# Performance work log

Measured on AMD Instinct MI355X. Metric: run time of the kernel, lower is better.

Reference implementation:

```python
import jax, jax.numpy as jnp
import numpy as np

EPS = 1e-06

def elu_feature_map(x):
    return jax.nn.elu(x) + 1.0

def setup_inputs() -> dict:
    key = jax.random.key(0)
    k1, k2, k3 = jax.random.split(key, 3)
    B, N, H, D = 4, 8192, 8, 64
    queries = jax.random.normal(k1, (B, N, H, D), dtype=jnp.float32)
    keys = jax.random.normal(k2, (B, N, H, D), dtype=jnp.float32)
    values = jax.random.normal(k3, (B, N, H, D), dtype=jnp.float32)
    key_lengths_mask = jnp.ones((B, N), dtype=jnp.float32)  # all keys valid
    return {"queries": queries, "keys": keys, "values": values,
            "key_lengths_mask": key_lengths_mask}

def reference(queries, keys, values, key_lengths_mask):
    # queries/keys/values: [B, N, H, D]; key_lengths_mask: [B, N]
    Q = elu_feature_map(queries)
    K = elu_feature_map(keys) * key_lengths_mask[:, :, None, None]
    # KV: [B, H, M, D] outer-product accumulation over sequence
    KV = jnp.einsum('bnhd,bnhm->bhmd', K, values)
    # normalizer Z: [B, N, H]
    Z = 1.0 / (jnp.einsum('bnhd,bhd->bnh', Q, K.sum(axis=1)) + EPS)
    # output V: [B, N, H, M]
    V = jnp.einsum('bnhd,bhmd,bnh->bnhm', Q, KV, Z)
    return V
```

## Files before the change

### kernel.cpp

```cpp
#include <hip/hip_runtime.h>

static constexpr int B = 4;
static constexpr int N = 8192;
static constexpr int H = 8;
static constexpr int BH = B * H;
#define EPSF 1e-6f

typedef _Float16 f16;
typedef _Float16 f16x8 __attribute__((ext_vector_type(8)));
typedef float f32x4 __attribute__((ext_vector_type(4)));

__device__ __forceinline__ float featmap(float x) {
    return x > 0.0f ? (x + 1.0f) : __expf(x);
}

union H8 { f16x8 v; unsigned long long u[2]; };
__device__ __forceinline__ f16x8 lds_load8(const f16* p) {
    H8 r;
    r.u[0] = *(const unsigned long long*)(p);
    r.u[1] = *(const unsigned long long*)(p + 4);
    return r.v;
}
__device__ __forceinline__ unsigned pack2(float a, float b) {
    union { f16 h[2]; unsigned u; } x;
    x.h[0] = (f16)a; x.h[1] = (f16)b;
    return x.u;
}
__device__ __forceinline__ unsigned long long pack4(float a, float b, float c, float d) {
    union { f16 h[4]; unsigned long long u; } x;
    x.h[0] = (f16)a; x.h[1] = (f16)b; x.h[2] = (f16)c; x.h[3] = (f16)d;
    return x.u;
}

static constexpr int S1 = 16;
static constexpr int ROWS1 = N / S1;
static constexpr int NSTEPS1 = ROWS1 / 32;

__global__ __launch_bounds__(256, 2) void kv_pass(
    const float* __restrict__ keys,
    const float* __restrict__ values,
    const float* __restrict__ mask,
    float* __restrict__ kv,
    float* __restrict__ ksum)
{
    const int bh = blockIdx.x, b = bh >> 3, h = bh & 7;
    const int t = threadIdx.x;
    const int wave = t >> 6, lane = t & 63;
    const int p = t >> 4;
    const int c = t & 15;
    const int quad = lane >> 4;
    const int l15 = lane & 15;
    const int n0 = blockIdx.y * ROWS1;

    __shared__ f16 KT[2][64][36];
    __shared__ f16 VT[2][64][36];
    __shared__ float Ksw[4][64];

    const float* mrow = mask + (size_t)b * N;

    int n = n0 + 2 * p;
    size_t g0 = ((size_t)((b * N + n) * H + h)) * 64 + c * 4;
    size_t g1 = g0 + (size_t)H * 64;
    float4 kq0 = *(const float4*)(keys + g0);
    float4 kq1 = *(const float4*)(keys + g1);
    float4 vq0 = *(const float4*)(values + g0);
    float4 vq1 = *(const float4*)(values + g1);
    float mk0 = mrow[n], mk1 = mrow[n + 1];

    f32x4 acc[4];
    #pragma unroll
    for (int i = 0; i < 4; ++i) acc[i] = (f32x4){0.f, 0.f, 0.f, 0.f};
    float ksacc[4] = {0.f, 0.f, 0.f, 0.f};

    for (int s = 0; s < NSTEPS1; ++s) {
        const int buf = s & 1;
        const float fk0[4] = {featmap(kq0.x) * mk0, featmap(kq0.y) * mk0,
                              featmap(kq0.z) * mk0, featmap(kq0.w) * mk0};
        const float fk1[4] = {featmap(kq1.x) * mk1, featmap(kq1.y) * mk1,
                              featmap(kq1.z) * mk1, featmap(kq1.w) * mk1};
        const float fv0[4] = {vq0.x, vq0.y, vq0.z, vq0.w};
        const float fv1[4] = {vq1.x, vq1.y, vq1.z, vq1.w};
        #pragma unroll
        for (int dd = 0; dd < 4; ++dd) {
            ksacc[dd] += fk0[dd] + fk1[dd];
            *(unsigned*)&KT[buf][c * 4 + dd][2 * p] = pack2(fk0[dd], fk1[dd]);
            *(unsigned*)&VT[buf][c * 4 + dd][2 * p] = pack2(fv0[dd], fv1[dd]);
        }
        if (s + 1 < NSTEPS1) {
            const int nn = n0 + (s + 1) * 32 + 2 * p;
            const size_t h0 = ((size_t)((b * N + nn) * H + h)) * 64 + c * 4;
            const size_t h1 = h0 + (size_t)H * 64;
            kq0 = *(const float4*)(keys + h0);
            kq1 = *(const float4*)(keys + h1);
            vq0 = *(const float4*)(values + h0);
            vq1 = *(const float4*)(values + h1);
            mk0 = mrow[nn]; mk1 = mrow[nn + 1];
        }
        __syncthreads();
        const f16x8 afr = lds_load8(&VT[buf][wave * 16 + l15][quad * 8]);
        #pragma unroll
        for (int dt = 0; dt < 4; ++dt) {
            const f16x8 bfr = lds_load8(&KT[buf][dt * 16 + l15][quad * 8]);
            acc[dt] = __builtin_amdgcn_mfma_f32_16x16x32_f16(afr, bfr, acc[dt], 0, 0, 0);
        }
    }

    float* kvb = kv + (size_t)bh * 4096;
    #pragma unroll
    for (int dt = 0; dt < 4; ++dt) {
        #pragma unroll
        for (int reg = 0; reg < 4; ++reg) {
            const int m = wave * 16 + quad * 4 + reg;
            atomicAdd(kvb + m * 64 + dt * 16 + l15, acc[dt][reg]);
        }
    }
    #pragma unroll
    for (int dd = 0; dd < 4; ++dd) {
        float v = ksacc[dd];
        v += __shfl_xor(v, 16);
        v += __shfl_xor(v, 32);
        if (lane < 16) Ksw[wave][lane * 4 + dd] = v;
    }
    __syncthreads();
    if (t < 64) {
        atomicAdd(ksum + bh * 64 + t, Ksw[0][t] + Ksw[1][t] + Ksw[2][t] + Ksw[3][t]);
    }
}

__global__ __launch_bounds__(256, 2) void out_pass(
    const float* __restrict__ queries,
    const float* __restrict__ kv,
    const float* __restrict__ ksum,
    float* __restrict__ out)
{
    const int bh = blockIdx.x, b = bh >> 3, h = bh & 7;
    const int t = threadIdx.x;
    const int wave = t >> 6, lane = t & 63;
    const int quad = lane >> 4;
    const int l15 = lane & 15;
    const int n0 = blockIdx.y * 256;

    __shared__ f16 Qsh[256][68];
    __shared__ f16 KVh[64][68];
    __shared__ float Ksh[64];

    #pragma unroll
    for (int l = 0; l < 4; ++l) {
        const int idx = t + l * 256;
        const int m = idx >> 4, cc = idx & 15;
        const float4 v = *(const float4*)(kv + (size_t)bh * 4096 + m * 64 + cc * 4);
        *(unsigned long long*)&KVh[m][cc * 4] = pack4(v.x, v.y, v.z, v.w);
    }
    if (t < 64) Ksh[t] = ksum[bh * 64 + t];

    #pragma unroll
    for (int l = 0; l < 16; ++l) {
        const int idx = t + l * 256;
        const int r = idx >> 4, cc = idx & 15;
        const int nn = n0 + r;
        const float4 q = *(const float4*)(queries + ((size_t)((b * N + nn) * H + h)) * 64 + cc * 4);
        *(unsigned long long*)&Qsh[r][cc * 4] =
            pack4(featmap(q.x), featmap(q.y), featmap(q.z), featmap(q.w));
    }
    __syncthreads();

    f16x8 bfr[4][2];
    #pragma unroll
    for (int mt = 0; mt < 4; ++mt)
        #pragma unroll
        for (int ks = 0; ks < 2; ++ks)
            bfr[mt][ks] = lds_load8(&KVh[mt * 16 + l15][ks * 32 + quad * 8]);
    f16x8 bz[2];
    #pragma unroll
    for (int ks = 0; ks < 2; ++ks) {
        #pragma unroll
        for (int j = 0; j < 8; ++j) {
            const float kval = Ksh[ks * 32 + quad * 8 + j];
            bz[ks][j] = (l15 == 0) ? (f16)kval : (f16)0.f;
        }
    }

    #pragma unroll
    for (int nt = 0; nt < 4; ++nt) {
        const int r0 = wave * 64 + nt * 16;
        f32x4 acc[4];
        #pragma unroll
        for (int i = 0; i < 4; ++i) acc[i] = (f32x4){0.f, 0.f, 0.f, 0.f};
        f32x4 az = (f32x4){0.f, 0.f, 0.f, 0.f};

        #pragma unroll
        for (int ks = 0; ks < 2; ++ks) {
            const f16x8 afr = lds_load8(&Qsh[r0 + l15][ks * 32 + quad * 8]);
            #pragma unroll
            for (int mt = 0; mt < 4; ++mt)
                acc[mt] = __builtin_amdgcn_mfma_f32_16x16x32_f16(afr, bfr[mt][ks], acc[mt], 0, 0, 0);
            az = __builtin_amdgcn_mfma_f32_16x16x32_f16(afr, bz[ks], az, 0, 0, 0);
        }

        #pragma unroll
        for (int reg = 0; reg < 4; ++reg) {
            const float den = __shfl(az[reg], lane & 48);
            const float zin = 1.0f / (den + EPSF);
            const int nn = n0 + r0 + quad * 4 + reg;
            float* op = out + ((size_t)((b * N + nn) * H + h)) * 64 + l15;
            #pragma unroll
            for (int mt = 0; mt < 4; ++mt)
                op[mt * 16] = acc[mt][reg] * zin;
        }
    }
}

extern "C" void kernel_launch(void* const* d_in, const int* in_sizes, int n_in,
                              void* d_out, int out_size, void* d_ws, size_t ws_size,
                              hipStream_t stream)
{
    const float* q    = (const float*)d_in[0];
    const float* k    = (const float*)d_in[1];
    const float* v    = (const float*)d_in[2];
    const float* mask = (const float*)d_in[3];
    float* out = (float*)d_out;

    float* kv = (float*)d_ws;
    float* ks = kv + (size_t)BH * 64 * 64;

    hipMemsetAsync(d_ws, 0, (size_t)(BH * 64 * 64 + BH * 64) * sizeof(float), stream);
    kv_pass<<<dim3(BH, S1), 256, 0, stream>>>(k, v, mask, kv, ks);
    out_pass<<<dim3(BH, 32), 256, 0, stream>>>(q, kv, ks, out);
}
```

Before: 229.6 us.

## Split kv_pass into more blocks and load out_pass operands directly into registers

```diff
diff --git a/kernel.cpp b/kernel.cpp
--- a/kernel.cpp
+++ b/kernel.cpp
@@ -26,17 +26,17 @@
     x.h[0] = (f16)a; x.h[1] = (f16)b;
     return x.u;
 }
-__device__ __forceinline__ unsigned long long pack4(float a, float b, float c, float d) {
-    union { f16 h[4]; unsigned long long u; } x;
-    x.h[0] = (f16)a; x.h[1] = (f16)b; x.h[2] = (f16)c; x.h[3] = (f16)d;
-    return x.u;
-}
-
-static constexpr int S1 = 16;
-static constexpr int ROWS1 = N / S1;
+__device__ __forceinline__ f16x8 pack8(const float4& a, const float4& b) {
+    f16x8 r;
+    r[0] = (f16)a.x; r[1] = (f16)a.y; r[2] = (f16)a.z; r[3] = (f16)a.w;
+    r[4] = (f16)b.x; r[5] = (f16)b.y; r[6] = (f16)b.z; r[7] = (f16)b.w;
+    return r;
+}
+
+static constexpr int ROWS1 = 256;
 static constexpr int NSTEPS1 = ROWS1 / 32;
 
-__global__ __launch_bounds__(256, 2) void kv_pass(
+__global__ __launch_bounds__(256, 4) void kv_pass(
     const float* __restrict__ keys,
     const float* __restrict__ values,
     const float* __restrict__ mask,
@@ -127,7 +127,7 @@
     }
 }
 
-__global__ __launch_bounds__(256, 2) void out_pass(
+__global__ __launch_bounds__(256, 4) void out_pass(
     const float* __restrict__ queries,
     const float* __restrict__ kv,
     const float* __restrict__ ksum,
@@ -136,72 +136,78 @@
     const int bh = blockIdx.x, b = bh >> 3, h = bh & 7;
     const int t = threadIdx.x;
     const int wave = t >> 6, lane = t & 63;
-    const int quad = lane >> 4;
-    const int l15 = lane & 15;
-    const int n0 = blockIdx.y * 256;
-
-    __shared__ f16 Qsh[256][68];
-    __shared__ f16 KVh[64][68];
-    __shared__ float Ksh[64];
-
-    #pragma unroll
-    for (int l = 0; l < 4; ++l) {
-        const int idx = t + l * 256;
-        const int m = idx >> 4, cc = idx & 15;
-        const float4 v = *(const float4*)(kv + (size_t)bh * 4096 + m * 64 + cc * 4);
-        *(unsigned long long*)&KVh[m][cc * 4] = pack4(v.x, v.y, v.z, v.w);
-    }
-    if (t < 64) Ksh[t] = ksum[bh * 64 + t];
-
-    #pragma unroll
-    for (int l = 0; l < 16; ++l) {
-        const int idx = t + l * 256;
-        const int r = idx >> 4, cc = idx & 15;
-        const int nn = n0 + r;
-        const float4 q = *(const float4*)(queries + ((size_t)((b * N + nn) * H + h)) * 64 + cc * 4);
-        *(unsigned long long*)&Qsh[r][cc * 4] =
-            pack4(featmap(q.x), featmap(q.y), featmap(q.z), featmap(q.w));
-    }
-    __syncthreads();
-
+    const int quad = lane >> 4, l15 = lane & 15;
+    const int n0 = blockIdx.y * 256 + wave * 64;
+
+    const float* kvb = kv + (size_t)bh * 4096;
     f16x8 bfr[4][2];
     #pragma unroll
-    for (int mt = 0; mt < 4; ++mt)
-        #pragma unroll
-        for (int ks = 0; ks < 2; ++ks)
-            bfr[mt][ks] = lds_load8(&KVh[mt * 16 + l15][ks * 32 + quad * 8]);
+    for (int mt = 0; mt < 4; ++mt) {
+        #pragma unroll
+        for (int ks = 0; ks < 2; ++ks) {
+            const float* p = kvb + (mt * 16 + l15) * 64 + ks * 32 + quad * 8;
+            const float4 x0 = *(const float4*)p;
+            const float4 x1 = *(const float4*)(p + 4);
+            bfr[mt][ks] = pack8(x0, x1);
+        }
+    }
     f16x8 bz[2];
     #pragma unroll
     for (int ks = 0; ks < 2; ++ks) {
-        #pragma unroll
-        for (int j = 0; j < 8; ++j) {
-            const float kval = Ksh[ks * 32 + quad * 8 + j];
-            bz[ks][j] = (l15 == 0) ? (f16)kval : (f16)0.f;
-        }
+        const float* zp = ksum + bh * 64 + ks * 32 + quad * 8;
+        const float4 z0 = *(const float4*)zp;
+        const float4 z1 = *(const float4*)(zp + 4);
+        const f16x8 zf = pack8(z0, z1);
+        #pragma unroll
+        for (int j = 0; j < 8; ++j)
+            bz[ks][j] = (l15 == 0) ? zf[j] : (f16)0.f;
+    }
+
+    const size_t rs = (size_t)H * 64;
+    const float* q0p = queries + ((size_t)((b * N + n0) + 0) * H + h) * 64;
+
+    float4 qa, qb, qc, qd;
+    {
+        const float* qp = q0p + (size_t)l15 * rs + quad * 8;
+        qa = *(const float4*)qp;       qb = *(const float4*)(qp + 4);
+        qc = *(const float4*)(qp + 32); qd = *(const float4*)(qp + 36);
     }
 
     #pragma unroll
     for (int nt = 0; nt < 4; ++nt) {
-        const int r0 = wave * 64 + nt * 16;
+        float4 fa, fb, fc, fd;
+        fa.x = featmap(qa.x); fa.y = featmap(qa.y); fa.z = featmap(qa.z); fa.w = featmap(qa.w);
+        fb.x = featmap(qb.x); fb.y = featmap(qb.y); fb.z = featmap(qb.z); fb.w = featmap(qb.w);
+        fc.x = featmap(qc.x); fc.y = featmap(qc.y); fc.z = featmap(qc.z); fc.w = featmap(qc.w);
+        fd.x = featmap(qd.x); fd.y = featmap(qd.y); fd.z = featmap(qd.z); fd.w = featmap(qd.w);
+        const f16x8 afr0 = pack8(fa, fb);
+        const f16x8 afr1 = pack8(fc, fd);
+
+        if (nt < 3) {
+            const float* qp = q0p + (size_t)((nt + 1) * 16 + l15) * rs + quad * 8;
+            qa = *(const float4*)qp;       qb = *(const float4*)(qp + 4);
+            qc = *(const float4*)(qp + 32); qd = *(const float4*)(qp + 36);
+        }
+
         f32x4 acc[4];
         #pragma unroll
         for (int i = 0; i < 4; ++i) acc[i] = (f32x4){0.f, 0.f, 0.f, 0.f};
         f32x4 az = (f32x4){0.f, 0.f, 0.f, 0.f};
 
         #pragma unroll
-        for (int ks = 0; ks < 2; ++ks) {
-            const f16x8 afr = lds_load8(&Qsh[r0 + l15][ks * 32 + quad * 8]);
-            #pragma unroll
-            for (int mt = 0; mt < 4; ++mt)
-                acc[mt] = __builtin_amdgcn_mfma_f32_16x16x32_f16(afr, bfr[mt][ks], acc[mt], 0, 0, 0);
-            az = __builtin_amdgcn_mfma_f32_16x16x32_f16(afr, bz[ks], az, 0, 0, 0);
-        }
+        for (int mt = 0; mt < 4; ++mt)
+            acc[mt] = __builtin_amdgcn_mfma_f32_16x16x32_f16(afr0, bfr[mt][0], acc[mt], 0, 0, 0);
+        az = __builtin_amdgcn_mfma_f32_16x16x32_f16(afr0, bz[0], az, 0, 0, 0);
+        #pragma unroll
+        for (int mt = 0; mt < 4; ++mt)
+            acc[mt] = __builtin_amdgcn_mfma_f32_16x16x32_f16(afr1, bfr[mt][1], acc[mt], 0, 0, 0);
+        az = __builtin_amdgcn_mfma_f32_16x16x32_f16(afr1, bz[1], az, 0, 0, 0);
 
         #pragma unroll
         for (int reg = 0; reg < 4; ++reg) {
             const float den = __shfl(az[reg], lane & 48);
             const float zin = 1.0f / (den + EPSF);
-            const int nn = n0 + r0 + quad * 4 + reg;
+            const int nn = n0 + nt * 16 + quad * 4 + reg;
             float* op = out + ((size_t)((b * N + nn) * H + h)) * 64 + l15;
             #pragma unroll
             for (int mt = 0; mt < 4; ++mt)
@@ -224,6 +230,6 @@
     float* ks = kv + (size_t)BH * 64 * 64;
 
     hipMemsetAsync(d_ws, 0, (size_t)(BH * 64 * 64 + BH * 64) * sizeof(float), stream);
-    kv_pass<<<dim3(BH, S1), 256, 0, stream>>>(k, v, mask, kv, ks);
+    kv_pass<<<dim3(BH, N / ROWS1), 256, 0, stream>>>(k, v, mask, kv, ks);
     out_pass<<<dim3(BH, 32), 256, 0, stream>>>(q, kv, ks, out);
 }
```

Result: slower. 242.6 us (+5.7%).
